# Kernel tuning notes

Hardware: AMD Instinct MI355X
Metric: run time of the kernel (lower is better)

The kernel has to match this reference:

```python
import jax, jax.numpy as jnp
import numpy as np
from jax import lax

N = 2048
BS = 64
NUM_ITR = 25


def setup_inputs() -> dict:
    key = jax.random.key(0)
    k1, k2, k3, k4, k5 = jax.random.split(key, 5)
    scale = 0.5 / np.sqrt(N)  # keep iteration matrices contractive so the recurrence stays bounded
    H = jax.random.normal(k1, (N, N), dtype=jnp.float32) / np.sqrt(N)
    Dinv = jax.random.normal(k2, (N, N), dtype=jnp.float32) * scale
    U = jax.random.normal(k3, (N, N), dtype=jnp.float32) * scale
    invM = jax.random.normal(k4, (N, N), dtype=jnp.float32) * scale
    y = jax.random.normal(k5, (BS, N), dtype=jnp.float32)
    return {"num_itr": NUM_ITR, "bs": BS, "y": y, "H": H, "Dinv": Dinv, "U": U, "invM": invM}


def reference(num_itr, bs, y, H, Dinv, U, invM):
    n = H.shape[0]
    s0 = jnp.zeros((bs, n), dtype=y.dtype)
    yMF = y @ H.T                 # [bs, n]
    s_init = yMF @ Dinv           # initial Gauss-Seidel estimate

    def step(s, _):
        s_next = (yMF - s @ U) @ invM
        return s_next, s_next

    s_final, traj_iters = lax.scan(step, s_init, None, length=num_itr)
    # traj matches the torch list: [zeros, s_1, ..., s_num_itr]
    traj = jnp.concatenate([s0[None], traj_iters], axis=0)  # [num_itr+1, bs, n]
    return s_final, traj
```

## Files before the change

kernel.cpp:

```cpp
#include <hip/hip_runtime.h>
#include <hip/hip_bf16.h>

#define NDIM 2048
#define BS   64
#define NITR 25
#define NM4  (NDIM * NDIM / 4)

typedef __bf16 bf16_t;
typedef __bf16 bf16x4 __attribute__((ext_vector_type(4)));
typedef __bf16 bf16x8 __attribute__((ext_vector_type(8)));
typedef float  f32x4  __attribute__((ext_vector_type(4)));

__global__ __launch_bounds__(256) void prep(
    const float* __restrict__ H, const float* __restrict__ U,
    const float* __restrict__ Dinv, const float* __restrict__ invM,
    const float* __restrict__ y,
    bf16_t* __restrict__ H16, bf16_t* __restrict__ U16,
    bf16_t* __restrict__ Dt, bf16_t* __restrict__ iMt,
    bf16_t* __restrict__ y16, float* __restrict__ traj0) {
  __shared__ bf16_t tile[32][33];
  int b = blockIdx.x, tid = threadIdx.x;
  if (b < 8192) {
    int idx = b * 256 + tid;
    const float* src = (idx < NM4) ? H : U;
    bf16_t* dst = (idx < NM4) ? H16 : U16;
    int i = (idx < NM4) ? idx : idx - NM4;
    float4 v = ((const float4*)src)[i];
    bf16x4 o = {(bf16_t)v.x, (bf16_t)v.y, (bf16_t)v.z, (bf16_t)v.w};
    ((bf16x4*)dst)[i] = o;
    if (idx < BS * NDIM / 4) {
      float4 w = ((const float4*)y)[idx];
      bf16x4 o2 = {(bf16_t)w.x, (bf16_t)w.y, (bf16_t)w.z, (bf16_t)w.w};
      ((bf16x4*)y16)[idx] = o2;
      ((float4*)traj0)[idx] = make_float4(0.f, 0.f, 0.f, 0.f);
    }
  } else {
    int id = b - 8192;
    int bx = id & 63, by = id >> 6;
    int tx = tid & 31, ty = tid >> 5;
    const float* src[2] = {Dinv, invM};
    bf16_t* dst[2] = {Dt, iMt};
#pragma unroll
    for (int m = 0; m < 2; ++m) {
      __syncthreads();
#pragma unroll
      for (int i = 0; i < 4; ++i)
        tile[ty + i * 8][tx] =
            (bf16_t)src[m][(size_t)(by * 32 + ty + i * 8) * NDIM + bx * 32 + tx];
      __syncthreads();
#pragma unroll
      for (int i = 0; i < 4; ++i)
        dst[m][(size_t)(bx * 32 + ty + i * 8) * NDIM + by * 32 + tx] = tile[tx][ty + i * 8];
    }
  }
}

__device__ __forceinline__ void skinny_role(
    const bf16_t* __restrict__ A, const bf16_t* __restrict__ Bt, int n0, char* smem,
    const float* __restrict__ add, float sign,
    float* o32, float* o32b, bf16_t* o16) {
  bf16x8* panel = (bf16x8*)smem;
  int tid = threadIdx.x, lane = tid & 63, wave = tid >> 6;
#pragma unroll
  for (int i = 0; i < 16; ++i) {
    int F = i * 256 + tid, c = F >> 6, ln = F & 63;
    panel[F] = *(const bf16x8*)(Bt + (size_t)(n0 + (ln & 15)) * NDIM + c * 32 + ((ln >> 4) << 3));
  }
  __syncthreads();
  int ml = lane & 15, q = lane >> 4;
  const bf16x8* Ap = (const bf16x8*)(A + (size_t)(wave * 16 + ml) * NDIM) + q;
  const bf16x8* Bp = panel + lane;
  f32x4 acc[4];
  acc[0] = acc[1] = acc[2] = acc[3] = (f32x4){0.f, 0.f, 0.f, 0.f};
#pragma unroll 16
  for (int c = 0; c < 64; ++c) {
    bf16x8 a = Ap[c * 4];
    bf16x8 b = Bp[c * 64];
    acc[c & 3] = __builtin_amdgcn_mfma_f32_16x16x32_bf16(a, b, acc[c & 3], 0, 0, 0);
  }
  f32x4 s = (acc[0] + acc[1]) + (acc[2] + acc[3]);
  int mrow = wave * 16 + q * 4, col = n0 + ml;
#pragma unroll
  for (int r = 0; r < 4; ++r) {
    size_t o = (size_t)(mrow + r) * NDIM + col;
    float v = sign * s[r];
    if (add) v += add[o];
    if (o32)  o32[o]  = v;
    if (o32b) o32b[o] = v;
    if (o16)  o16[o]  = (bf16_t)v;
  }
}

__device__ __forceinline__ void wgemm_role(
    const bf16_t* __restrict__ A, const bf16_t* __restrict__ Bt,
    bf16_t* __restrict__ C, int blk, char* smem) {
  bf16x8* As = (bf16x8*)smem;
  bf16x8* Bs = (bf16x8*)(smem + 8192);
  int tid = threadIdx.x, lane = tid & 63, wave = tid >> 6;
  int m0 = (blk >> 4) * 128, n0 = (blk & 15) * 128;
  int wr16 = (wave >> 1) * 4, wc16 = (wave & 1) * 4;
  int ml = lane & 15, q = lane >> 4;

  f32x4 acc[4][4];
#pragma unroll
  for (int i = 0; i < 4; ++i)
#pragma unroll
    for (int j = 0; j < 4; ++j) acc[i][j] = (f32x4){0.f, 0.f, 0.f, 0.f};

  for (int k0 = 0; k0 < NDIM; k0 += 32) {
    __syncthreads();
#pragma unroll
    for (int i = 0; i < 2; ++i) {
      int S = i * 256 + tid, g = S >> 6, ln = S & 63;
      int row = g * 16 + (ln & 15), kq = (ln >> 4) << 3;
      As[S] = *(const bf16x8*)(A  + (size_t)(m0 + row) * NDIM + k0 + kq);
      Bs[S] = *(const bf16x8*)(Bt + (size_t)(n0 + row) * NDIM + k0 + kq);
    }
    __syncthreads();
    bf16x8 af[4], bfr[4];
#pragma unroll
    for (int i = 0; i < 4; ++i) {
      af[i]  = As[(wr16 + i) * 64 + lane];
      bfr[i] = Bs[(wc16 + i) * 64 + lane];
    }
#pragma unroll
    for (int i = 0; i < 4; ++i)
#pragma unroll
      for (int j = 0; j < 4; ++j)
        acc[i][j] = __builtin_amdgcn_mfma_f32_16x16x32_bf16(af[i], bfr[j], acc[i][j], 0, 0, 0);
  }
  int wr = wr16 * 16, wc = wc16 * 16;
#pragma unroll
  for (int i = 0; i < 4; ++i)
#pragma unroll
    for (int j = 0; j < 4; ++j)
#pragma unroll
      for (int r = 0; r < 4; ++r)
        C[(size_t)(m0 + wr + i * 16 + q * 4 + r) * NDIM + n0 + wc + j * 16 + ml] =
            (bf16_t)acc[i][j][r];
}

__global__ __launch_bounds__(256) void mega1(
    const bf16_t* __restrict__ U16, const bf16_t* __restrict__ iMt16,
    const bf16_t* __restrict__ y16, const bf16_t* __restrict__ H16,
    bf16_t* __restrict__ Wrm, bf16_t* __restrict__ Wt, bf16_t* __restrict__ yMF16) {
  __shared__ char smem[65536];
  int b = blockIdx.x;
  if (b < 128)
    skinny_role(y16, H16, b * 16, smem, nullptr, 1.f, nullptr, nullptr, yMF16);
  else if (b < 384)
    wgemm_role(U16, iMt16, Wrm, b - 128, smem);
  else
    wgemm_role(iMt16, U16, Wt, b - 384, smem);
}

__global__ __launch_bounds__(256) void mega2(
    const bf16_t* __restrict__ Wt, const bf16_t* __restrict__ Wrm,
    const bf16_t* __restrict__ yMF16, const bf16_t* __restrict__ iMt16,
    const bf16_t* __restrict__ Dt16,
    bf16_t* __restrict__ W2t, float* __restrict__ c32, bf16_t* __restrict__ c16,
    bf16_t* __restrict__ zA) {
  __shared__ char smem[65536];
  int b = blockIdx.x;
  if (b < 128)
    skinny_role(yMF16, iMt16, b * 16, smem, nullptr, 1.f, c32, nullptr, c16);
  else if (b < 256)
    skinny_role(yMF16, Dt16, (b - 128) * 16, smem, nullptr, 1.f, nullptr, nullptr, zA);
  else
    wgemm_role(Wt, Wrm, W2t, b - 256, smem);
}

__global__ __launch_bounds__(256) void skinny_dual(
    const bf16_t* __restrict__ A0, const bf16_t* __restrict__ A1,
    const bf16_t* __restrict__ Bt, const float* __restrict__ add, float sign,
    float* o32_0, float* o32_1, float* o32b_1,
    bf16_t* o16_0, bf16_t* o16_1) {
  __shared__ char smem[65536];
  int b = blockIdx.x, p = b >> 1, mh = b & 1;
  skinny_role(mh ? A1 : A0, Bt, p * 16, smem, add, sign,
              mh ? o32_1 : o32_0, mh ? o32b_1 : nullptr, mh ? o16_1 : o16_0);
}

extern "C" void kernel_launch(void* const* d_in, const int* in_sizes, int n_in,
                              void* d_out, int out_size, void* d_ws, size_t ws_size,
                              hipStream_t stream) {
  const float* y    = (const float*)d_in[2];
  const float* H    = (const float*)d_in[3];
  const float* Dinv = (const float*)d_in[4];
  const float* U    = (const float*)d_in[5];
  const float* invM = (const float*)d_in[6];

  float* out     = (float*)d_out;
  float* s_final = out;
  float* traj    = out + BS * NDIM;

  char* ws = (char*)d_ws;
  size_t off = 0;
  auto alloc = [&](size_t bytes) -> void* {
    void* p = ws + off;
    off += (bytes + 255) & ~(size_t)255;
    return p;
  };
  bf16_t* U16   = (bf16_t*)alloc((size_t)NDIM * NDIM * 2);
  bf16_t* Dt16  = (bf16_t*)alloc((size_t)NDIM * NDIM * 2);
  bf16_t* iMt16 = (bf16_t*)alloc((size_t)NDIM * NDIM * 2);
  bf16_t* H16   = (bf16_t*)alloc((size_t)NDIM * NDIM * 2);
  bf16_t* Wrm   = (bf16_t*)alloc((size_t)NDIM * NDIM * 2);
  bf16_t* Wt    = (bf16_t*)alloc((size_t)NDIM * NDIM * 2);
  bf16_t* y16   = (bf16_t*)alloc((size_t)BS * NDIM * 2);
  bf16_t* yMF16 = (bf16_t*)alloc((size_t)BS * NDIM * 2);
  bf16_t* c16   = (bf16_t*)alloc((size_t)BS * NDIM * 2);
  float*  c32   = (float*)alloc((size_t)BS * NDIM * 4);
  float*  c2_32 = (float*)alloc((size_t)BS * NDIM * 4);
  bf16_t* zA    = (bf16_t*)alloc((size_t)2 * BS * NDIM * 2);
  bf16_t* zB    = (bf16_t*)alloc((size_t)2 * BS * NDIM * 2);
  bf16_t* W2t   = H16;

  prep<<<12288, 256, 0, stream>>>(H, U, Dinv, invM, y, H16, U16, Dt16, iMt16, y16, traj);
  mega1<<<640, 256, 0, stream>>>(U16, iMt16, y16, H16, Wrm, Wt, yMF16);
  mega2<<<512, 256, 0, stream>>>(Wt, Wrm, yMF16, iMt16, Dt16, W2t, c32, c16, zA);
  skinny_dual<<<256, 256, 0, stream>>>(c16, zA, Wt, c32, -1.f,
                                       c2_32, traj + (size_t)BS * NDIM, nullptr,
                                       nullptr, zA + (size_t)64 * NDIM);
  bf16_t* zcur = zA;
  bf16_t* znxt = zB;
  for (int j = 1; j <= 12; ++j) {
    skinny_dual<<<256, 256, 0, stream>>>(
        zcur, zcur + (size_t)64 * NDIM, W2t, c2_32, 1.f,
        traj + (size_t)(2 * j) * BS * NDIM, traj + (size_t)(2 * j + 1) * BS * NDIM,
        (j == 12) ? s_final : nullptr,
        znxt, znxt + (size_t)64 * NDIM);
    bf16_t* tmp = zcur; zcur = znxt; znxt = tmp;
  }
}
```

Before: 425.5 us.

## Extend recurrence to four-step stride using squared iteration matrix W^4

```diff
diff --git a/kernel.cpp b/kernel.cpp
--- a/kernel.cpp
+++ b/kernel.cpp
@@ -3,8 +3,8 @@
 
 #define NDIM 2048
 #define BS   64
-#define NITR 25
 #define NM4  (NDIM * NDIM / 4)
+#define BSN  ((size_t)BS * NDIM)
 
 typedef __bf16 bf16_t;
 typedef __bf16 bf16x4 __attribute__((ext_vector_type(4)));
@@ -61,22 +61,27 @@
     float* o32, float* o32b, bf16_t* o16) {
   bf16x8* panel = (bf16x8*)smem;
   int tid = threadIdx.x, lane = tid & 63, wave = tid >> 6;
-#pragma unroll
-  for (int i = 0; i < 16; ++i) {
-    int F = i * 256 + tid, c = F >> 6, ln = F & 63;
-    panel[F] = *(const bf16x8*)(Bt + (size_t)(n0 + (ln & 15)) * NDIM + c * 32 + ((ln >> 4) << 3));
-  }
-  __syncthreads();
   int ml = lane & 15, q = lane >> 4;
-  const bf16x8* Ap = (const bf16x8*)(A + (size_t)(wave * 16 + ml) * NDIM) + q;
-  const bf16x8* Bp = panel + lane;
   f32x4 acc[4];
   acc[0] = acc[1] = acc[2] = acc[3] = (f32x4){0.f, 0.f, 0.f, 0.f};
+#pragma unroll
+  for (int half = 0; half < 2; ++half) {
+    __syncthreads();
+#pragma unroll
+    for (int i = 0; i < 8; ++i) {
+      int F = i * 256 + tid, c = F >> 6, ln = F & 63;
+      panel[F] = *(const bf16x8*)(Bt + (size_t)(n0 + (ln & 15)) * NDIM +
+                                  half * 1024 + c * 32 + ((ln >> 4) << 3));
+    }
+    __syncthreads();
+    const bf16x8* Ap = (const bf16x8*)(A + (size_t)(wave * 16 + ml) * NDIM) + q + half * 128;
+    const bf16x8* Bp = panel + lane;
 #pragma unroll 16
-  for (int c = 0; c < 64; ++c) {
-    bf16x8 a = Ap[c * 4];
-    bf16x8 b = Bp[c * 64];
-    acc[c & 3] = __builtin_amdgcn_mfma_f32_16x16x32_bf16(a, b, acc[c & 3], 0, 0, 0);
+    for (int c = 0; c < 32; ++c) {
+      bf16x8 a = Ap[c * 4];
+      bf16x8 b = Bp[c * 64];
+      acc[c & 3] = __builtin_amdgcn_mfma_f32_16x16x32_bf16(a, b, acc[c & 3], 0, 0, 0);
+    }
   }
   f32x4 s = (acc[0] + acc[1]) + (acc[2] + acc[3]);
   int mrow = wave * 16 + q * 4, col = n0 + ml;
@@ -97,88 +102,140 @@
   bf16x8* As = (bf16x8*)smem;
   bf16x8* Bs = (bf16x8*)(smem + 8192);
   int tid = threadIdx.x, lane = tid & 63, wave = tid >> 6;
-  int m0 = (blk >> 4) * 128, n0 = (blk & 15) * 128;
-  int wr16 = (wave >> 1) * 4, wc16 = (wave & 1) * 4;
+  int m0 = (blk >> 5) * 128, n0 = (blk & 31) * 64;
+  int wr4 = (wave >> 1) * 4, wc2 = (wave & 1) * 2;
   int ml = lane & 15, q = lane >> 4;
 
-  f32x4 acc[4][4];
+  f32x4 acc[4][2];
 #pragma unroll
   for (int i = 0; i < 4; ++i)
 #pragma unroll
-    for (int j = 0; j < 4; ++j) acc[i][j] = (f32x4){0.f, 0.f, 0.f, 0.f};
+    for (int j = 0; j < 2; ++j) acc[i][j] = (f32x4){0.f, 0.f, 0.f, 0.f};
 
   for (int k0 = 0; k0 < NDIM; k0 += 32) {
     __syncthreads();
 #pragma unroll
     for (int i = 0; i < 2; ++i) {
       int S = i * 256 + tid, g = S >> 6, ln = S & 63;
-      int row = g * 16 + (ln & 15), kq = (ln >> 4) << 3;
-      As[S] = *(const bf16x8*)(A  + (size_t)(m0 + row) * NDIM + k0 + kq);
-      Bs[S] = *(const bf16x8*)(Bt + (size_t)(n0 + row) * NDIM + k0 + kq);
-    }
-    __syncthreads();
-    bf16x8 af[4], bfr[4];
-#pragma unroll
-    for (int i = 0; i < 4; ++i) {
-      af[i]  = As[(wr16 + i) * 64 + lane];
-      bfr[i] = Bs[(wc16 + i) * 64 + lane];
-    }
+      As[S] = *(const bf16x8*)(A + (size_t)(m0 + g * 16 + (ln & 15)) * NDIM + k0 + ((ln >> 4) << 3));
+    }
+    {
+      int S = tid, g = S >> 6, ln = S & 63;
+      Bs[S] = *(const bf16x8*)(Bt + (size_t)(n0 + g * 16 + (ln & 15)) * NDIM + k0 + ((ln >> 4) << 3));
+    }
+    __syncthreads();
+    bf16x8 af[4], bfr[2];
+#pragma unroll
+    for (int i = 0; i < 4; ++i) af[i] = As[(wr4 + i) * 64 + lane];
+#pragma unroll
+    for (int j = 0; j < 2; ++j) bfr[j] = Bs[(wc2 + j) * 64 + lane];
 #pragma unroll
     for (int i = 0; i < 4; ++i)
 #pragma unroll
-      for (int j = 0; j < 4; ++j)
+      for (int j = 0; j < 2; ++j)
         acc[i][j] = __builtin_amdgcn_mfma_f32_16x16x32_bf16(af[i], bfr[j], acc[i][j], 0, 0, 0);
   }
-  int wr = wr16 * 16, wc = wc16 * 16;
+  int wr = wr4 * 16, wc = wc2 * 16;
 #pragma unroll
   for (int i = 0; i < 4; ++i)
 #pragma unroll
-    for (int j = 0; j < 4; ++j)
+    for (int j = 0; j < 2; ++j)
 #pragma unroll
       for (int r = 0; r < 4; ++r)
         C[(size_t)(m0 + wr + i * 16 + q * 4 + r) * NDIM + n0 + wc + j * 16 + ml] =
             (bf16_t)acc[i][j][r];
 }
 
-__global__ __launch_bounds__(256) void mega1(
+__device__ __forceinline__ void transpose_role(const bf16_t* __restrict__ src,
+                                               bf16_t* __restrict__ dst, int blk, char* smem) {
+  bf16_t (*tile)[72] = (bf16_t(*)[72])smem;
+  int tid = threadIdx.x;
+  int bx = blk & 31, by = blk >> 5;
+#pragma unroll
+  for (int i = 0; i < 2; ++i) {
+    int v = i * 256 + tid, r = v >> 3, c8 = (v & 7) * 8;
+    *(bf16x8*)&tile[r][c8] = *(const bf16x8*)(src + (size_t)(by * 64 + r) * NDIM + bx * 64 + c8);
+  }
+  __syncthreads();
+#pragma unroll
+  for (int i = 0; i < 2; ++i) {
+    int v = i * 256 + tid, r = v >> 3, c8 = (v & 7) * 8;
+    bf16x8 o;
+#pragma unroll
+    for (int j = 0; j < 8; ++j) o[j] = tile[c8 + j][r];
+    *(bf16x8*)(dst + (size_t)(bx * 64 + r) * NDIM + by * 64 + c8) = o;
+  }
+}
+
+__global__ __launch_bounds__(256) void megaA(
     const bf16_t* __restrict__ U16, const bf16_t* __restrict__ iMt16,
     const bf16_t* __restrict__ y16, const bf16_t* __restrict__ H16,
-    bf16_t* __restrict__ Wrm, bf16_t* __restrict__ Wt, bf16_t* __restrict__ yMF16) {
-  __shared__ char smem[65536];
-  int b = blockIdx.x;
-  if (b < 128)
-    skinny_role(y16, H16, b * 16, smem, nullptr, 1.f, nullptr, nullptr, yMF16);
-  else if (b < 384)
-    wgemm_role(U16, iMt16, Wrm, b - 128, smem);
-  else
-    wgemm_role(iMt16, U16, Wt, b - 384, smem);
-}
-
-__global__ __launch_bounds__(256) void mega2(
+    bf16_t* __restrict__ Wrm, bf16_t* __restrict__ yMF16) {
+  __shared__ char smem[32768];
+  int b = blockIdx.x;
+  if (b < 128) skinny_role(y16, H16, b * 16, smem, nullptr, 1.f, nullptr, nullptr, yMF16);
+  else         wgemm_role(U16, iMt16, Wrm, b - 128, smem);
+}
+
+__global__ __launch_bounds__(256) void megaB(
+    const bf16_t* __restrict__ Wrm, const bf16_t* __restrict__ yMF16,
+    const bf16_t* __restrict__ iMt16, const bf16_t* __restrict__ Dt16,
+    bf16_t* __restrict__ Wt, float* __restrict__ c32, bf16_t* __restrict__ c16,
+    bf16_t* __restrict__ z0) {
+  __shared__ char smem[32768];
+  int b = blockIdx.x;
+  if (b < 1024)      transpose_role(Wrm, Wt, b, smem);
+  else if (b < 1152) skinny_role(yMF16, iMt16, (b - 1024) * 16, smem, nullptr, 1.f, c32, nullptr, c16);
+  else               skinny_role(yMF16, Dt16, (b - 1152) * 16, smem, nullptr, 1.f, nullptr, nullptr, z0);
+}
+
+__global__ __launch_bounds__(256) void megaC(
     const bf16_t* __restrict__ Wt, const bf16_t* __restrict__ Wrm,
-    const bf16_t* __restrict__ yMF16, const bf16_t* __restrict__ iMt16,
-    const bf16_t* __restrict__ Dt16,
-    bf16_t* __restrict__ W2t, float* __restrict__ c32, bf16_t* __restrict__ c16,
+    const bf16_t* __restrict__ z0, const bf16_t* __restrict__ c16,
+    const float* __restrict__ c32,
+    bf16_t* __restrict__ W2t, float* __restrict__ traj1, bf16_t* __restrict__ z0b,
+    float* __restrict__ c2_32, bf16_t* __restrict__ c2_16) {
+  __shared__ char smem[32768];
+  int b = blockIdx.x;
+  if (b < 512)      wgemm_role(Wt, Wrm, W2t, b, smem);
+  else if (b < 640) skinny_role(z0, Wt, (b - 512) * 16, smem, c32, -1.f, traj1, nullptr, z0b);
+  else              skinny_role(c16, Wt, (b - 640) * 16, smem, c32, -1.f, c2_32, nullptr, c2_16);
+}
+
+__global__ __launch_bounds__(256) void megaD(
+    const bf16_t* __restrict__ W2t, const bf16_t* __restrict__ z0,
+    const bf16_t* __restrict__ c2_16, const float* __restrict__ c2_32,
+    bf16_t* __restrict__ W2rm, float* __restrict__ traj2, float* __restrict__ traj3,
+    bf16_t* __restrict__ zA, float* __restrict__ c4_32) {
+  __shared__ char smem[32768];
+  int b = blockIdx.x;
+  if (b < 1024)      transpose_role(W2t, W2rm, b, smem);
+  else if (b < 1152) skinny_role(z0, W2t, (b - 1024) * 16, smem, c2_32, 1.f, traj2, nullptr, zA);
+  else if (b < 1280) skinny_role(z0 + BSN, W2t, (b - 1152) * 16, smem, c2_32, 1.f, traj3, nullptr, zA + BSN);
+  else               skinny_role(c2_16, W2t, (b - 1280) * 16, smem, c2_32, 1.f, c4_32, nullptr, nullptr);
+}
+
+__global__ __launch_bounds__(256) void megaE(
+    const bf16_t* __restrict__ W2t, const bf16_t* __restrict__ W2rm,
+    const bf16_t* __restrict__ zA_in, const float* __restrict__ c2_32,
+    bf16_t* __restrict__ W4t, float* __restrict__ traj4, float* __restrict__ traj5,
     bf16_t* __restrict__ zA) {
-  __shared__ char smem[65536];
-  int b = blockIdx.x;
-  if (b < 128)
-    skinny_role(yMF16, iMt16, b * 16, smem, nullptr, 1.f, c32, nullptr, c16);
-  else if (b < 256)
-    skinny_role(yMF16, Dt16, (b - 128) * 16, smem, nullptr, 1.f, nullptr, nullptr, zA);
-  else
-    wgemm_role(Wt, Wrm, W2t, b - 256, smem);
-}
-
-__global__ __launch_bounds__(256) void skinny_dual(
-    const bf16_t* __restrict__ A0, const bf16_t* __restrict__ A1,
-    const bf16_t* __restrict__ Bt, const float* __restrict__ add, float sign,
-    float* o32_0, float* o32_1, float* o32b_1,
-    bf16_t* o16_0, bf16_t* o16_1) {
-  __shared__ char smem[65536];
-  int b = blockIdx.x, p = b >> 1, mh = b & 1;
-  skinny_role(mh ? A1 : A0, Bt, p * 16, smem, add, sign,
-              mh ? o32_1 : o32_0, mh ? o32b_1 : nullptr, mh ? o16_1 : o16_0);
+  __shared__ char smem[32768];
+  int b = blockIdx.x;
+  if (b < 512)      wgemm_role(W2t, W2rm, W4t, b, smem);
+  else if (b < 640) skinny_role(zA_in, W2t, (b - 512) * 16, smem, c2_32, 1.f, traj4, nullptr, zA + 2 * BSN);
+  else              skinny_role(zA_in + BSN, W2t, (b - 640) * 16, smem, c2_32, 1.f, traj5, nullptr, zA + 3 * BSN);
+}
+
+__global__ __launch_bounds__(256) void quad_step(
+    const bf16_t* __restrict__ zin, const bf16_t* __restrict__ W4t,
+    const float* __restrict__ c4_32, float* __restrict__ trajb,
+    bf16_t* __restrict__ zout, float* __restrict__ sfin) {
+  __shared__ char smem[32768];
+  int b = blockIdx.x, ci = b & 3, p = b >> 2;
+  skinny_role(zin + (size_t)ci * BSN, W4t, p * 16, smem, c4_32, 1.f,
+              trajb + (size_t)ci * BSN, (ci == 3) ? sfin : nullptr,
+              zout + (size_t)ci * BSN);
 }
 
 extern "C" void kernel_launch(void* const* d_in, const int* in_sizes, int n_in,
@@ -192,7 +249,7 @@
 
   float* out     = (float*)d_out;
   float* s_final = out;
-  float* traj    = out + BS * NDIM;
+  float* traj    = out + BSN;
 
   char* ws = (char*)d_ws;
   size_t off = 0;
@@ -207,29 +264,34 @@
   bf16_t* H16   = (bf16_t*)alloc((size_t)NDIM * NDIM * 2);
   bf16_t* Wrm   = (bf16_t*)alloc((size_t)NDIM * NDIM * 2);
   bf16_t* Wt    = (bf16_t*)alloc((size_t)NDIM * NDIM * 2);
-  bf16_t* y16   = (bf16_t*)alloc((size_t)BS * NDIM * 2);
-  bf16_t* yMF16 = (bf16_t*)alloc((size_t)BS * NDIM * 2);
-  bf16_t* c16   = (bf16_t*)alloc((size_t)BS * NDIM * 2);
-  float*  c32   = (float*)alloc((size_t)BS * NDIM * 4);
-  float*  c2_32 = (float*)alloc((size_t)BS * NDIM * 4);
-  bf16_t* zA    = (bf16_t*)alloc((size_t)2 * BS * NDIM * 2);
-  bf16_t* zB    = (bf16_t*)alloc((size_t)2 * BS * NDIM * 2);
+  bf16_t* y16   = (bf16_t*)alloc(BSN * 2);
+  bf16_t* yMF16 = (bf16_t*)alloc(BSN * 2);
+  bf16_t* c16   = (bf16_t*)alloc(BSN * 2);
+  bf16_t* c2_16 = (bf16_t*)alloc(BSN * 2);
+  float*  c32   = (float*)alloc(BSN * 4);
+  float*  c2_32 = (float*)alloc(BSN * 4);
+  float*  c4_32 = (float*)alloc(BSN * 4);
+  bf16_t* z0    = (bf16_t*)alloc(2 * BSN * 2);
+  bf16_t* zA    = (bf16_t*)alloc(4 * BSN * 2);
+  bf16_t* zB    = (bf16_t*)alloc(4 * BSN * 2);
   bf16_t* W2t   = H16;
+  bf16_t* W2rm  = U16;
+  bf16_t* W4t   = Dt16;
 
   prep<<<12288, 256, 0, stream>>>(H, U, Dinv, invM, y, H16, U16, Dt16, iMt16, y16, traj);
-  mega1<<<640, 256, 0, stream>>>(U16, iMt16, y16, H16, Wrm, Wt, yMF16);
-  mega2<<<512, 256, 0, stream>>>(Wt, Wrm, yMF16, iMt16, Dt16, W2t, c32, c16, zA);
-  skinny_dual<<<256, 256, 0, stream>>>(c16, zA, Wt, c32, -1.f,
-                                       c2_32, traj + (size_t)BS * NDIM, nullptr,
-                                       nullptr, zA + (size_t)64 * NDIM);
+  megaA<<<640, 256, 0, stream>>>(U16, iMt16, y16, H16, Wrm, yMF16);
+  megaB<<<1280, 256, 0, stream>>>(Wrm, yMF16, iMt16, Dt16, Wt, c32, c16, z0);
+  megaC<<<768, 256, 0, stream>>>(Wt, Wrm, z0, c16, c32, W2t, traj + BSN, z0 + BSN, c2_32, c2_16);
+  megaD<<<1408, 256, 0, stream>>>(W2t, z0, c2_16, c2_32, W2rm, traj + 2 * BSN, traj + 3 * BSN,
+                                  zA, c4_32);
+  megaE<<<768, 256, 0, stream>>>(W2t, W2rm, zA, c2_32, W4t, traj + 4 * BSN, traj + 5 * BSN, zA);
+
   bf16_t* zcur = zA;
   bf16_t* znxt = zB;
-  for (int j = 1; j <= 12; ++j) {
-    skinny_dual<<<256, 256, 0, stream>>>(
-        zcur, zcur + (size_t)64 * NDIM, W2t, c2_32, 1.f,
-        traj + (size_t)(2 * j) * BS * NDIM, traj + (size_t)(2 * j + 1) * BS * NDIM,
-        (j == 12) ? s_final : nullptr,
-        znxt, znxt + (size_t)64 * NDIM);
+  for (int g = 0; g < 5; ++g) {
+    float* sfin = (g == 4) ? s_final : nullptr;
+    quad_step<<<512, 256, 0, stream>>>(zcur, W4t, c4_32, traj + (size_t)(6 + 4 * g) * BSN,
+                                       znxt, sfin);
     bf16_t* tmp = zcur; zcur = znxt; znxt = tmp;
   }
 }
```

After: 449.6 us. 1.06x slower.
